# Optimization experiments

Measured on AMD Instinct MI355X. Metric: run time of the kernel, lower is better.

Reference implementation:

```python
import jax, jax.numpy as jnp
import numpy as np


def setup_inputs() -> dict:
    key = jax.random.key(0)
    k1, k2, k3, k4 = jax.random.split(key, 4)
    L, d, n_tokens = 4096, 2048, 4096
    x = jax.random.normal(k1, (L, d), dtype=jnp.float32)
    Wq_w = jax.random.normal(k2, (d, d), dtype=jnp.float32) * (1.0 / np.sqrt(d))
    Pk = jax.random.normal(k3, (1, n_tokens, d), dtype=jnp.float32)
    Pv = jax.random.normal(k4, (1, n_tokens, d), dtype=jnp.float32)
    return {"x": x, "Wq_w": Wq_w, "Pk": Pk, "Pv": Pv, "sliding_window_size": 1024}


def reference(x, Wq_w, Pk, Pv, sliding_window_size):
    # x: (L, d); Pk/Pv: (1, n_tokens, d). Single-head cross attention to a
    # fixed parameter token bank with a bidirectional sliding-window mask
    # |q_idx - kv_idx| < sliding_window_size (flex_attention semantics,
    # default scale = 1/sqrt(d)).
    L, d = x.shape
    n_tokens = Pk.shape[1]
    scale = 1.0 / np.sqrt(d).astype(np.float32)

    q = x @ Wq_w.T                                    # (L, d)
    scores = jnp.einsum('ld,td->lt', q, Pk[0]) * scale  # (L, n_tokens)

    q_idx = jnp.arange(L)[:, None]
    kv_idx = jnp.arange(n_tokens)[None, :]
    mask = jnp.abs(q_idx - kv_idx) < sliding_window_size  # (L, n_tokens)

    neg_inf = jnp.asarray(jnp.finfo(scores.dtype).min, scores.dtype)
    probs = jax.nn.softmax(jnp.where(mask, scores, neg_inf), axis=-1)
    y = jnp.einsum('lt,td->ld', probs, Pv[0])         # (L, d)
    return y[None, :, :]                              # (1, L, d) after squeeze(1)
```

## Files before the change

kernel.cpp:

```cpp
#include <hip/hip_runtime.h>


using bf16x8 = __attribute__((ext_vector_type(8))) short;
using f32x4  = __attribute__((ext_vector_type(4))) float;

#define LDIM 4096
#define TDIM 4096
#define DDIM 2048

static __device__ __forceinline__ unsigned short f2bf(float f) {
  union { float f; unsigned u; } c; c.f = f;
  unsigned r = c.u + 0x7FFFu + ((c.u >> 16) & 1u);
  return (unsigned short)(r >> 16);
}
static __device__ __forceinline__ unsigned pack2(float a, float b) {
  return (unsigned)f2bf(a) | ((unsigned)f2bf(b) << 16);
}
static __device__ __forceinline__ void gload16(const void* g, void* l) {
  __builtin_amdgcn_global_load_lds((const __attribute__((address_space(1))) void*)g,
                                   (__attribute__((address_space(3))) void*)l, 16, 0, 0);
}

__global__ __launch_bounds__(256) void k_prep(const float* __restrict__ x,
                                              const float* __restrict__ Wq,
                                              const float* __restrict__ Pk,
                                              const float* __restrict__ Pv,
                                              unsigned short* __restrict__ xb,
                                              unsigned short* __restrict__ wb,
                                              unsigned short* __restrict__ kb,
                                              unsigned short* __restrict__ vt,
                                              float* __restrict__ rowsum) {
  const int tid = threadIdx.x;
  const int b = blockIdx.x;
  if (b < 10240) {
    const float* in; unsigned short* out; size_t i;
    if (b < 4096)      { in = x;  out = xb; i = (size_t)b * 256 + tid; }
    else if (b < 6144) { in = Wq; out = wb; i = (size_t)(b - 4096) * 256 + tid; }
    else               { in = Pk; out = kb; i = (size_t)(b - 6144) * 256 + tid; }
    const float4* p = (const float4*)(in + i * 8);
    float4 a = p[0], c = p[1];
    uint4 o = { pack2(a.x, a.y), pack2(a.z, a.w), pack2(c.x, c.y), pack2(c.z, c.w) };
    *(uint4*)(out + i * 8) = o;
    return;
  }
  if (b == 12288) {
    for (int k = tid; k < LDIM; k += 256) rowsum[k] = 0.f;
    return;
  }
  __shared__ unsigned short tile[64][72];
  const int b2 = b - 10240;
  const int t0 = (b2 & 63) * 64, j0 = (b2 >> 6) * 64;
  const int r = tid >> 4, c4 = (tid & 15) * 4;
#pragma unroll
  for (int rr = 0; rr < 64; rr += 16) {
    float4 v = *(const float4*)(Pv + (size_t)(t0 + r + rr) * DDIM + j0 + c4);
    tile[c4 + 0][r + rr] = f2bf(v.x);
    tile[c4 + 1][r + rr] = f2bf(v.y);
    tile[c4 + 2][r + rr] = f2bf(v.z);
    tile[c4 + 3][r + rr] = f2bf(v.w);
  }
  __syncthreads();
  const int jr = tid >> 3, tc = (tid & 7) * 8;
#pragma unroll
  for (int jj = 0; jj < 64; jj += 32)
    *(uint4*)(vt + (size_t)(j0 + jr + jj) * TDIM + t0 + tc) =
        *(const uint4*)&tile[jr + jj][tc];
}

static __device__ __forceinline__ void gemm_loop(const unsigned short* __restrict__ A,
                                                 const unsigned short* __restrict__ B,
                                                 int m0, int n0, long lda, long ldb,
                                                 int kbeg, int kend,
                                                 unsigned short* As, unsigned short* Bs,
                                                 f32x4 (&acc)[4][4]) {
  const int tid = threadIdx.x;
  const int wave = tid >> 6, lane = tid & 63;
  const int quad = lane >> 4, l16 = lane & 15;
  const int wm = wave >> 1, wn = wave & 1;
  const int srow = wave * 32 + (lane >> 2);
  const int scb  = (lane & 3) ^ ((lane >> 4) & 3);
  const int fu   = (l16 >> 2) & 3;

  const unsigned short* gA = A + (long)(m0 + srow) * lda + scb * 8;
  const unsigned short* gB = B + (long)(n0 + srow) * ldb + scb * 8;
  unsigned short* lA = As + wave * 1024;
  unsigned short* lB = Bs + wave * 1024;

  for (int k0 = kbeg; k0 < kend; k0 += 32) {
    gload16(gA + k0,            lA);
    gload16(gA + k0 + 16 * lda, lA + 512);
    gload16(gB + k0,            lB);
    gload16(gB + k0 + 16 * ldb, lB + 512);
    __syncthreads();
    bf16x8 af[4], bfr[4];
#pragma unroll
    for (int i = 0; i < 4; i++)
      af[i] = *(const bf16x8*)&As[(wm * 64 + i * 16 + l16) * 32 + ((quad ^ fu) * 8)];
#pragma unroll
    for (int j = 0; j < 4; j++)
      bfr[j] = *(const bf16x8*)&Bs[(wn * 64 + j * 16 + l16) * 32 + ((quad ^ fu) * 8)];
#pragma unroll
    for (int i = 0; i < 4; i++)
#pragma unroll
      for (int j = 0; j < 4; j++)
        acc[i][j] = __builtin_amdgcn_mfma_f32_16x16x32_bf16(af[i], bfr[j], acc[i][j], 0, 0, 0);
    __syncthreads();
  }
}

__global__ __launch_bounds__(256) void k1_qgemm(const unsigned short* __restrict__ X,
                                                const unsigned short* __restrict__ W,
                                                unsigned short* __restrict__ q) {
  __shared__ __align__(16) unsigned short As[128 * 32];
  __shared__ __align__(16) unsigned short Bs[128 * 32];
  f32x4 acc[4][4] = {};
  const int m0 = blockIdx.y * 128, n0 = blockIdx.x * 128;
  gemm_loop(X, W, m0, n0, DDIM, DDIM, 0, DDIM, As, Bs, acc);
  const int tid = threadIdx.x;
  const int wave = tid >> 6, lane = tid & 63;
  const int quad = lane >> 4, l16 = lane & 15, wm = wave >> 1, wn = wave & 1;
#pragma unroll
  for (int i = 0; i < 4; i++)
#pragma unroll
    for (int j = 0; j < 4; j++)
#pragma unroll
      for (int r = 0; r < 4; r++) {
        int row = m0 + wm * 64 + i * 16 + quad * 4 + r;
        int col = n0 + wn * 64 + j * 16 + l16;
        q[(long)row * DDIM + col] = f2bf(acc[i][j][r]);
      }
}

__global__ __launch_bounds__(256) void k2_qk(const unsigned short* __restrict__ Q,
                                             const unsigned short* __restrict__ Kb,
                                             unsigned short* __restrict__ P,
                                             float* __restrict__ rowsum,
                                             const int* __restrict__ wptr) {
  const int w = *wptr;
  const int l0 = blockIdx.y * 128, t0 = blockIdx.x * 128;
  int lo = l0 - w + 1; if (lo < 0) lo = 0;
  int hi = l0 + 127 + w - 1; if (hi > TDIM - 1) hi = TDIM - 1;
  if ((int)blockIdx.x < (lo >> 7) || (int)blockIdx.x > (hi >> 7)) return;
  __shared__ __align__(16) unsigned short As[128 * 32];
  __shared__ __align__(16) unsigned short Bs[128 * 32];
  f32x4 acc[4][4] = {};
  gemm_loop(Q, Kb, l0, t0, DDIM, DDIM, 0, DDIM, As, Bs, acc);
  const float scale = 0.022097086912079608f;
  const int tid = threadIdx.x;
  const int wave = tid >> 6, lane = tid & 63;
  const int quad = lane >> 4, l16 = lane & 15, wm = wave >> 1, wn = wave & 1;
#pragma unroll
  for (int i = 0; i < 4; i++) {
    float rs[4] = {0.f, 0.f, 0.f, 0.f};
#pragma unroll
    for (int j = 0; j < 4; j++)
#pragma unroll
      for (int r = 0; r < 4; r++) {
        int l = l0 + wm * 64 + i * 16 + quad * 4 + r;
        int t = t0 + wn * 64 + j * 16 + l16;
        int dlt = l - t; dlt = dlt < 0 ? -dlt : dlt;
        float e = 0.f;
        if (dlt < w) e = __expf(acc[i][j][r] * scale);
        unsigned short bv = f2bf(e);
        P[(long)l * TDIM + t] = bv;
        rs[r] += __uint_as_float((unsigned)bv << 16);
      }
#pragma unroll
    for (int r = 0; r < 4; ++r) {
      float s = rs[r];
      s += __shfl_xor(s, 1);
      s += __shfl_xor(s, 2);
      s += __shfl_xor(s, 4);
      s += __shfl_xor(s, 8);
      if (l16 == 0) atomicAdd(&rowsum[l0 + wm * 64 + i * 16 + quad * 4 + r], s);
    }
  }
}

__global__ __launch_bounds__(256) void k3_pv(const unsigned short* __restrict__ P,
                                             const unsigned short* __restrict__ Vt,
                                             const float* __restrict__ rowsum,
                                             float* __restrict__ Y,
                                             const int* __restrict__ wptr) {
  const int w = *wptr;
  const int l0 = blockIdx.y * 128, j0 = blockIdx.x * 128;
  int lo = l0 - w + 1; if (lo < 0) lo = 0;
  int hi = l0 + 127 + w - 1; if (hi > TDIM - 1) hi = TDIM - 1;
  const int kb = (lo >> 7) * 128, ke = ((hi >> 7) + 1) * 128;
  __shared__ __align__(16) unsigned short As[128 * 32];
  __shared__ __align__(16) unsigned short Bs[128 * 32];
  f32x4 acc[4][4] = {};
  gemm_loop(P, Vt, l0, j0, TDIM, TDIM, kb, ke, As, Bs, acc);
  const int tid = threadIdx.x;
  const int wave = tid >> 6, lane = tid & 63;
  const int quad = lane >> 4, l16 = lane & 15, wm = wave >> 1, wn = wave & 1;
#pragma unroll
  for (int i = 0; i < 4; i++)
#pragma unroll
    for (int r = 0; r < 4; r++) {
      const int l = l0 + wm * 64 + i * 16 + quad * 4 + r;
      const float inv = 1.0f / rowsum[l];
#pragma unroll
      for (int j = 0; j < 4; j++)
        Y[(long)l * DDIM + j0 + wn * 64 + j * 16 + l16] = acc[i][j][r] * inv;
    }
}

extern "C" void kernel_launch(void* const* d_in, const int* in_sizes, int n_in,
                              void* d_out, int out_size, void* d_ws, size_t ws_size,
                              hipStream_t stream) {
  const float* x  = (const float*)d_in[0];
  const float* Wq = (const float*)d_in[1];
  const float* Pk = (const float*)d_in[2];
  const float* Pv = (const float*)d_in[3];
  const int* wptr = (const int*)d_in[4];
  float* Y = (float*)d_out;

  unsigned short* base = (unsigned short*)d_ws;
  unsigned short* Pm = base;
  unsigned short* xb = base;
  unsigned short* wb = base + (size_t)LDIM * DDIM;
  unsigned short* kb = base + (size_t)TDIM * TDIM;
  unsigned short* vt = kb + (size_t)TDIM * DDIM;
  unsigned short* qb = vt + (size_t)DDIM * TDIM;
  float* rowsum = (float*)(qb + (size_t)LDIM * DDIM);

  k_prep<<<12289, 256, 0, stream>>>(x, Wq, Pk, Pv, xb, wb, kb, vt, rowsum);
  k1_qgemm<<<dim3(DDIM / 128, LDIM / 128), 256, 0, stream>>>(xb, wb, qb);
  k2_qk<<<dim3(TDIM / 128, LDIM / 128), 256, 0, stream>>>(qb, kb, Pm, rowsum, wptr);
  k3_pv<<<dim3(DDIM / 128, LDIM / 128), 256, 0, stream>>>(Pm, vt, rowsum, Y, wptr);
}
```

Measured before the change: 313.1 us.

## Double-buffer LDS tiles in shared GEMM loop to overlap loads with MFMA

Adds a second LDS buffer for the A and B tiles in the common GEMM loop. The first tile is loaded before the loop, and each iteration issues the global-to-LDS loads for the next k-step before running the MFMAs on the current buffer, leaving one barrier per iteration instead of two. The goal is to hide global load latency behind matrix math in all three GEMM kernels. LDS use per block doubles to 32 KB, which may lower occupancy. Because the async global_load_lds writes are not explicitly waited on before the barrier, correctness depends on the compiler inserting the vmcnt wait.

```diff
diff --git a/kernel.cpp b/kernel.cpp
--- a/kernel.cpp
+++ b/kernel.cpp
@@ -7,6 +7,8 @@
 #define LDIM 4096
 #define TDIM 4096
 #define DDIM 2048
+
+#define BUFE 4096
 
 static __device__ __forceinline__ unsigned short f2bf(float f) {
   union { float f; unsigned u; } c; c.f = f;
@@ -86,33 +88,43 @@
   unsigned short* lA = As + wave * 1024;
   unsigned short* lB = Bs + wave * 1024;
 
+  gload16(gA + kbeg,            lA);
+  gload16(gA + kbeg + 16 * lda, lA + 512);
+  gload16(gB + kbeg,            lB);
+  gload16(gB + kbeg + 16 * ldb, lB + 512);
+  __syncthreads();
+
+  int co = 0;
   for (int k0 = kbeg; k0 < kend; k0 += 32) {
-    gload16(gA + k0,            lA);
-    gload16(gA + k0 + 16 * lda, lA + 512);
-    gload16(gB + k0,            lB);
-    gload16(gB + k0 + 16 * ldb, lB + 512);
-    __syncthreads();
+    const int no = co ^ BUFE;
+    if (k0 + 32 < kend) {
+      gload16(gA + k0 + 32,            lA + no);
+      gload16(gA + k0 + 32 + 16 * lda, lA + no + 512);
+      gload16(gB + k0 + 32,            lB + no);
+      gload16(gB + k0 + 32 + 16 * ldb, lB + no + 512);
+    }
     bf16x8 af[4], bfr[4];
 #pragma unroll
     for (int i = 0; i < 4; i++)
-      af[i] = *(const bf16x8*)&As[(wm * 64 + i * 16 + l16) * 32 + ((quad ^ fu) * 8)];
+      af[i] = *(const bf16x8*)&As[co + (wm * 64 + i * 16 + l16) * 32 + ((quad ^ fu) * 8)];
 #pragma unroll
     for (int j = 0; j < 4; j++)
-      bfr[j] = *(const bf16x8*)&Bs[(wn * 64 + j * 16 + l16) * 32 + ((quad ^ fu) * 8)];
+      bfr[j] = *(const bf16x8*)&Bs[co + (wn * 64 + j * 16 + l16) * 32 + ((quad ^ fu) * 8)];
 #pragma unroll
     for (int i = 0; i < 4; i++)
 #pragma unroll
       for (int j = 0; j < 4; j++)
         acc[i][j] = __builtin_amdgcn_mfma_f32_16x16x32_bf16(af[i], bfr[j], acc[i][j], 0, 0, 0);
     __syncthreads();
+    co = no;
   }
 }
 
 __global__ __launch_bounds__(256) void k1_qgemm(const unsigned short* __restrict__ X,
                                                 const unsigned short* __restrict__ W,
                                                 unsigned short* __restrict__ q) {
-  __shared__ __align__(16) unsigned short As[128 * 32];
-  __shared__ __align__(16) unsigned short Bs[128 * 32];
+  __shared__ __align__(16) unsigned short As[2 * BUFE];
+  __shared__ __align__(16) unsigned short Bs[2 * BUFE];
   f32x4 acc[4][4] = {};
   const int m0 = blockIdx.y * 128, n0 = blockIdx.x * 128;
   gemm_loop(X, W, m0, n0, DDIM, DDIM, 0, DDIM, As, Bs, acc);
@@ -141,8 +153,8 @@
   int lo = l0 - w + 1; if (lo < 0) lo = 0;
   int hi = l0 + 127 + w - 1; if (hi > TDIM - 1) hi = TDIM - 1;
   if ((int)blockIdx.x < (lo >> 7) || (int)blockIdx.x > (hi >> 7)) return;
-  __shared__ __align__(16) unsigned short As[128 * 32];
-  __shared__ __align__(16) unsigned short Bs[128 * 32];
+  __shared__ __align__(16) unsigned short As[2 * BUFE];
+  __shared__ __align__(16) unsigned short Bs[2 * BUFE];
   f32x4 acc[4][4] = {};
   gemm_loop(Q, Kb, l0, t0, DDIM, DDIM, 0, DDIM, As, Bs, acc);
   const float scale = 0.022097086912079608f;
@@ -187,8 +199,8 @@
   int lo = l0 - w + 1; if (lo < 0) lo = 0;
   int hi = l0 + 127 + w - 1; if (hi > TDIM - 1) hi = TDIM - 1;
   const int kb = (lo >> 7) * 128, ke = ((hi >> 7) + 1) * 128;
-  __shared__ __align__(16) unsigned short As[128 * 32];
-  __shared__ __align__(16) unsigned short Bs[128 * 32];
+  __shared__ __align__(16) unsigned short As[2 * BUFE];
+  __shared__ __align__(16) unsigned short Bs[2 * BUFE];
   f32x4 acc[4][4] = {};
   gemm_loop(P, Vt, l0, j0, TDIM, TDIM, kb, ke, As, Bs, acc);
   const int tid = threadIdx.x;
```

New measurement: 319.8 us. 2.1% more time.

## Triple-buffer LDS in shared GEMM loop to overlap global loads with MFMA

Applied to the files above, without the earlier changes.

Replaces the single-buffered load/sync/compute/sync GEMM loop with a three-stage LDS ring buffer. Global-to-LDS loads for slab k+2 are issued before computing slab k, with vmcnt waits and a single barrier per iteration. The aim is to hide global memory latency behind MFMA work and drop one barrier per iteration. LDS per block triples to 48KB, which may lower occupancy.

```diff
diff --git a/kernel.cpp b/kernel.cpp
--- a/kernel.cpp
+++ b/kernel.cpp
@@ -7,6 +7,8 @@
 #define LDIM 4096
 #define TDIM 4096
 #define DDIM 2048
+
+#define BUFE 4096
 
 static __device__ __forceinline__ unsigned short f2bf(float f) {
   union { float f; unsigned u; } c; c.f = f;
@@ -86,33 +88,57 @@
   unsigned short* lA = As + wave * 1024;
   unsigned short* lB = Bs + wave * 1024;
 
-  for (int k0 = kbeg; k0 < kend; k0 += 32) {
-    gload16(gA + k0,            lA);
-    gload16(gA + k0 + 16 * lda, lA + 512);
-    gload16(gB + k0,            lB);
-    gload16(gB + k0 + 16 * ldb, lB + 512);
-    __syncthreads();
-    bf16x8 af[4], bfr[4];
-#pragma unroll
-    for (int i = 0; i < 4; i++)
-      af[i] = *(const bf16x8*)&As[(wm * 64 + i * 16 + l16) * 32 + ((quad ^ fu) * 8)];
-#pragma unroll
-    for (int j = 0; j < 4; j++)
-      bfr[j] = *(const bf16x8*)&Bs[(wn * 64 + j * 16 + l16) * 32 + ((quad ^ fu) * 8)];
-#pragma unroll
-    for (int i = 0; i < 4; i++)
-#pragma unroll
-      for (int j = 0; j < 4; j++)
-        acc[i][j] = __builtin_amdgcn_mfma_f32_16x16x32_bf16(af[i], bfr[j], acc[i][j], 0, 0, 0);
-    __syncthreads();
-  }
+#define STAGE(k0, bo) do {                                   \
+    gload16(gA + (k0),            lA + (bo));                \
+    gload16(gA + (k0) + 16 * lda, lA + (bo) + 512);          \
+    gload16(gB + (k0),            lB + (bo));                \
+    gload16(gB + (k0) + 16 * ldb, lB + (bo) + 512); } while (0)
+
+#define COMPUTE(co) do {                                                                     \
+    bf16x8 af[4], bfr[4];                                                                    \
+    _Pragma("unroll")                                                                        \
+    for (int i = 0; i < 4; i++)                                                              \
+      af[i] = *(const bf16x8*)&As[(co) + (wm * 64 + i * 16 + l16) * 32 + ((quad ^ fu) * 8)]; \
+    _Pragma("unroll")                                                                        \
+    for (int j = 0; j < 4; j++)                                                              \
+      bfr[j] = *(const bf16x8*)&Bs[(co) + (wn * 64 + j * 16 + l16) * 32 + ((quad ^ fu) * 8)];\
+    _Pragma("unroll")                                                                        \
+    for (int i = 0; i < 4; i++)                                                              \
+      _Pragma("unroll")                                                                      \
+      for (int j = 0; j < 4; j++)                                                            \
+        acc[i][j] = __builtin_amdgcn_mfma_f32_16x16x32_bf16(af[i], bfr[j], acc[i][j], 0, 0, 0); \
+  } while (0)
+
+  const int nslab = (kend - kbeg) >> 5;
+  STAGE(kbeg, 0);
+  STAGE(kbeg + 32, BUFE);
+  int co = 0, so = 2 * BUFE;
+  int kpre = kbeg + 64;
+  for (int it = 0; it < nslab - 2; ++it) {
+    asm volatile("s_waitcnt vmcnt(4)" ::: "memory");
+    __builtin_amdgcn_s_barrier();
+    STAGE(kpre, so);
+    kpre += 32;
+    COMPUTE(co);
+    co += BUFE; if (co == 3 * BUFE) co = 0;
+    so += BUFE; if (so == 3 * BUFE) so = 0;
+  }
+  asm volatile("s_waitcnt vmcnt(4)" ::: "memory");
+  __builtin_amdgcn_s_barrier();
+  COMPUTE(co);
+  co += BUFE; if (co == 3 * BUFE) co = 0;
+  asm volatile("s_waitcnt vmcnt(0)" ::: "memory");
+  __builtin_amdgcn_s_barrier();
+  COMPUTE(co);
+#undef STAGE
+#undef COMPUTE
 }
 
 __global__ __launch_bounds__(256) void k1_qgemm(const unsigned short* __restrict__ X,
                                                 const unsigned short* __restrict__ W,
                                                 unsigned short* __restrict__ q) {
-  __shared__ __align__(16) unsigned short As[128 * 32];
-  __shared__ __align__(16) unsigned short Bs[128 * 32];
+  __shared__ __align__(16) unsigned short As[3 * BUFE];
+  __shared__ __align__(16) unsigned short Bs[3 * BUFE];
   f32x4 acc[4][4] = {};
   const int m0 = blockIdx.y * 128, n0 = blockIdx.x * 128;
   gemm_loop(X, W, m0, n0, DDIM, DDIM, 0, DDIM, As, Bs, acc);
@@ -141,8 +167,8 @@
   int lo = l0 - w + 1; if (lo < 0) lo = 0;
   int hi = l0 + 127 + w - 1; if (hi > TDIM - 1) hi = TDIM - 1;
   if ((int)blockIdx.x < (lo >> 7) || (int)blockIdx.x > (hi >> 7)) return;
-  __shared__ __align__(16) unsigned short As[128 * 32];
-  __shared__ __align__(16) unsigned short Bs[128 * 32];
+  __shared__ __align__(16) unsigned short As[3 * BUFE];
+  __shared__ __align__(16) unsigned short Bs[3 * BUFE];
   f32x4 acc[4][4] = {};
   gemm_loop(Q, Kb, l0, t0, DDIM, DDIM, 0, DDIM, As, Bs, acc);
   const float scale = 0.022097086912079608f;
@@ -187,8 +213,8 @@
   int lo = l0 - w + 1; if (lo < 0) lo = 0;
   int hi = l0 + 127 + w - 1; if (hi > TDIM - 1) hi = TDIM - 1;
   const int kb = (lo >> 7) * 128, ke = ((hi >> 7) + 1) * 128;
-  __shared__ __align__(16) unsigned short As[128 * 32];
-  __shared__ __align__(16) unsigned short Bs[128 * 32];
+  __shared__ __align__(16) unsigned short As[3 * BUFE];
+  __shared__ __align__(16) unsigned short Bs[3 * BUFE];
   f32x4 acc[4][4] = {};
   gemm_loop(P, Vt, l0, j0, TDIM, TDIM, kb, ke, As, Bs, acc);
   const int tid = threadIdx.x;
```

After: 361.3 us. +15.4%, slower.
